# Kernel optimization log

Measured on AMD Instinct MI355X. Metric: run time of the kernel, lower is better.

The kernel has to match this reference:

```python
import jax, jax.numpy as jnp
import numpy as np

N_NODES = 100000
N_EDGES = 1600000
IN_DIM, HID_DIM, OUT_DIM = 128, 64, 64


def setup_inputs() -> dict:
    key = jax.random.key(0)
    ks = jax.random.split(key, 8)
    x = jax.random.normal(ks[0], (N_NODES, IN_DIM), dtype=jnp.float32)
    edge_index = jax.random.randint(ks[1], (2, N_EDGES), 0, N_NODES, dtype=jnp.int32)
    edge_weight = jax.random.uniform(ks[2], (N_EDGES,), dtype=jnp.float32)
    # GCNConv parameters (glorot-ish init)
    w1 = jax.random.normal(ks[3], (IN_DIM, HID_DIM), dtype=jnp.float32) / np.sqrt(IN_DIM)
    b1 = jnp.zeros((HID_DIM,), dtype=jnp.float32)
    w2 = jax.random.normal(ks[4], (HID_DIM, OUT_DIM), dtype=jnp.float32) / np.sqrt(HID_DIM)
    b2 = jnp.zeros((OUT_DIM,), dtype=jnp.float32)
    return {"x": x, "edge_index": edge_index, "edge_weight": edge_weight,
            "w1": w1, "b1": b1, "w2": w2, "b2": b2}


def _gcn_conv(h, src, dst, edge_weight, w, b, n_nodes):
    # GCNConv(normalize=False): linear transform, then edge-weighted scatter-add
    # (source_to_target flow: gather from src, scatter-sum into dst), then bias.
    h = h @ w                                   # [N, out]
    msg = h[src] * edge_weight[:, None]          # [E, out] irregular gather
    agg = jax.ops.segment_sum(msg, dst, num_segments=n_nodes)  # [N, out]
    return agg + b


def reference(x, edge_index, edge_weight, w1, b1, w2, b2):
    src, dst = edge_index[0], edge_index[1]
    n = x.shape[0]
    # Dropout is identity in eval mode (training=False).
    h = _gcn_conv(x, src, dst, edge_weight, w1, b1, n)
    h = jax.nn.relu(h)
    out = _gcn_conv(h, src, dst, edge_weight, w2, b2, n)
    return out
```

## Files before the change

### kernel.cpp

```cpp
#include <hip/hip_runtime.h>
#include <hip/hip_bf16.h>


#define N_NODES 100000
#define N_EDGES 1600000
#define NB1     391
#define T1      3072
#define NT1     521
#define CAP1    4706
#define GB1     782

typedef unsigned short ushort_t;
typedef unsigned int uint_t;
typedef __attribute__((ext_vector_type(8))) short bf16x8;
typedef __attribute__((ext_vector_type(4))) float floatx4;
typedef __attribute__((ext_vector_type(8))) ushort_t ushort8v;

static __device__ __forceinline__ float bf2f(ushort_t h) {
    return __uint_as_float(((uint_t)h) << 16);
}
static __device__ __forceinline__ ushort_t f2bf(float f) {
    uint_t u = __float_as_uint(f);
    u = (u + 0x7FFF + ((u >> 16) & 1)) >> 16;
    return (ushort_t)u;
}

__global__ __launch_bounds__(512) void k_init(int* __restrict__ gcursor)
{
    int t = threadIdx.x;
    if (t < NB1) gcursor[t] = t * CAP1;
}

__global__ __launch_bounds__(512) void k_p1g1(
    const int* __restrict__ src, const int* __restrict__ dst,
    const float* __restrict__ ew, int* __restrict__ gcursor,
    int2* __restrict__ recs1, int E,
    const float* __restrict__ X, const float* __restrict__ W,
    ushort_t* __restrict__ Y, int N)
{
    __shared__ __align__(16) char smem[37056];
    const int tid = threadIdx.x;

    if (blockIdx.x < NT1) {
        int* cnt     = (int*)smem;
        int* start   = cnt + NB1;
        int* cursor  = start + NB1;
        int* gb      = cursor + NB1;
        int* wsum    = (int*)(smem + 6256);
        int* wexc    = wsum + 8;
        int2* stg    = (int2*)(smem + 6336);
        ushort_t* sb = (ushort_t*)(smem + 30912);
        const int t = tid, b = blockIdx.x;
        const int lane = t & 63, wv = t >> 6;

        if (t < NB1) cnt[t] = 0;
        __syncthreads();
        const int e0 = b * T1;
        const int e1 = min(E, e0 + T1);
        for (int e = e0 + t; e < e1; e += 512)
            atomicAdd(&cnt[dst[e] >> 8], 1);
        __syncthreads();

        const int v = (t < NB1) ? cnt[t] : 0;
        int x = v;
        #pragma unroll
        for (int off = 1; off < 64; off <<= 1) {
            int y = __shfl_up(x, off);
            if (lane >= off) x += y;
        }
        if (lane == 63) wsum[wv] = x;
        __syncthreads();
        if (t < 8) {
            int w  = wsum[t];
            int xx = w;
            #pragma unroll
            for (int off = 1; off < 8; off <<= 1) {
                int y = __shfl_up(xx, off);
                if (t >= off) xx += y;
            }
            wexc[t] = xx - w;
        }
        __syncthreads();
        if (t < NB1) {
            int st = x + wexc[wv] - v;
            start[t]  = st;
            cursor[t] = st;
            gb[t]     = atomicAdd(&gcursor[t], v);
        }
        __syncthreads();

        for (int e = e0 + t; e < e1; e += 512) {
            int d  = dst[e];
            int bk = d >> 8;
            int p  = atomicAdd(&cursor[bk], 1);
            int2 r;
            r.x = ((d & 255) << 17) | src[e];
            r.y = __float_as_int(ew[e]);
            stg[p] = r;
            sb[p]  = (ushort_t)bk;
        }
        __syncthreads();
        const int n = e1 - e0;
        for (int i = t; i < n; i += 512) {
            int bk = sb[i];
            recs1[gb[bk] + (i - start[bk])] = stg[i];
        }
    } else {
        ushort_t* sA = (ushort_t*)smem;
        ushort_t* sB = (ushort_t*)(smem + 18432);
        const int b    = blockIdx.x - NT1;
        const int row0 = b * 128;

        for (int i = tid; i < 128 * 16; i += 512) {
            int k = i >> 4, n4 = (i & 15) * 4;
            float4 v = *(const float4*)(W + (size_t)k * 64 + n4);
            sB[(n4 + 0) * 136 + k] = f2bf(v.x);
            sB[(n4 + 1) * 136 + k] = f2bf(v.y);
            sB[(n4 + 2) * 136 + k] = f2bf(v.z);
            sB[(n4 + 3) * 136 + k] = f2bf(v.w);
        }
        for (int i = tid; i < 128 * 16; i += 512) {
            int r = i >> 4, c4 = (i & 15) * 4;
            int rg = row0 + r; if (rg > N - 1) rg = N - 1;
            float4 v = *(const float4*)(X + (size_t)rg * 128 + c4);
            *(ushort4*)(sA + r * 72 + c4) =
                make_ushort4(f2bf(v.x), f2bf(v.y), f2bf(v.z), f2bf(v.w));
        }
        __syncthreads();

        const int wid = tid >> 6, lane = tid & 63;
        const int m = lane & 15, quad = lane >> 4;
        floatx4 acc[4] = {};

        #pragma unroll
        for (int ksl = 0; ksl < 2; ++ksl) {
            bf16x8 a = *(const bf16x8*)(sA + (wid * 16 + m) * 72 + ksl * 32 + quad * 8);
            #pragma unroll
            for (int nt = 0; nt < 4; ++nt) {
                bf16x8 bfr = *(const bf16x8*)(sB + (nt * 16 + m) * 136 + ksl * 32 + quad * 8);
                acc[nt] = __builtin_amdgcn_mfma_f32_16x16x32_bf16(a, bfr, acc[nt], 0, 0, 0);
            }
        }
        __syncthreads();
        for (int i = tid; i < 128 * 16; i += 512) {
            int r = i >> 4, c4 = (i & 15) * 4;
            int rg = row0 + r; if (rg > N - 1) rg = N - 1;
            float4 v = *(const float4*)(X + (size_t)rg * 128 + 64 + c4);
            *(ushort4*)(sA + r * 72 + c4) =
                make_ushort4(f2bf(v.x), f2bf(v.y), f2bf(v.z), f2bf(v.w));
        }
        __syncthreads();
        #pragma unroll
        for (int ksl = 0; ksl < 2; ++ksl) {
            bf16x8 a = *(const bf16x8*)(sA + (wid * 16 + m) * 72 + ksl * 32 + quad * 8);
            #pragma unroll
            for (int nt = 0; nt < 4; ++nt) {
                bf16x8 bfr = *(const bf16x8*)(sB + (nt * 16 + m) * 136 + 64 + ksl * 32 + quad * 8);
                acc[nt] = __builtin_amdgcn_mfma_f32_16x16x32_bf16(a, bfr, acc[nt], 0, 0, 0);
            }
        }
        __syncthreads();
        #pragma unroll
        for (int nt = 0; nt < 4; ++nt)
            #pragma unroll
            for (int r = 0; r < 4; ++r)
                sA[(wid * 16 + quad * 4 + r) * 72 + nt * 16 + m] = f2bf(acc[nt][r]);
        __syncthreads();
        for (int i = tid; i < 128 * 8; i += 512) {
            int rr = i >> 3, c8 = (i & 7) * 8;
            int rg = row0 + rr;
            if (rg < N)
                *(ushort8v*)(Y + (size_t)rg * 64 + c8) =
                    *(const ushort8v*)(sA + rr * 72 + c8);
        }
    }
}

__global__ __launch_bounds__(1024) void k_pass2(
    const int2* __restrict__ recs1, const int* __restrict__ gcursor,
    int2* __restrict__ recs2, int2* __restrict__ nodeinfo, int N)
{
    __shared__ int cnt[256];
    __shared__ int s[256];
    __shared__ int cursor[256];
    const int t = threadIdx.x, b = blockIdx.x;
    const int lo = b * CAP1;
    const int hi = gcursor[b];

    if (t < 256) cnt[t] = 0;
    __syncthreads();
    for (int j = lo + t; j < hi; j += 1024)
        atomicAdd(&cnt[((uint_t)recs1[j].x) >> 17], 1);
    __syncthreads();
    const int v = (t < 256) ? cnt[t] : 0;
    if (t < 256) s[t] = v;
    #pragma unroll
    for (int off = 1; off < 256; off <<= 1) {
        __syncthreads();
        int a = (t >= off && t < 256) ? s[t - off] : 0;
        __syncthreads();
        if (t < 256) s[t] += a;
    }
    __syncthreads();
    if (t < 256) {
        const int stl = s[t] - v;
        cursor[t] = stl;
        const int ng = b * 256 + t;
        if (ng < N) {
            int2 ni; ni.x = lo + stl; ni.y = v;
            nodeinfo[ng] = ni;
        }
    }
    __syncthreads();
    for (int j = lo + t; j < hi; j += 1024) {
        int2 r = recs1[j];
        int dl = ((uint_t)r.x) >> 17;
        int p  = atomicAdd(&cursor[dl], 1);
        int2 o;
        o.x = r.x & 0x1FFFF;
        o.y = r.y;
        recs2[lo + p] = o;
    }
}

__global__ __launch_bounds__(256) void k_gemm2(
    const ushort_t* __restrict__ X, const float* __restrict__ W,
    ushort_t* __restrict__ Y, int N)
{
    __shared__ ushort_t sA[64 * 72];
    __shared__ ushort_t sB[64 * 72];
    const int tid  = threadIdx.x;
    const int row0 = blockIdx.x * 64;

    for (int i = tid; i < 64 * 16; i += 256) {
        int r = i >> 4, c4 = (i & 15) * 4;
        int rg = row0 + r; if (rg > N - 1) rg = N - 1;
        *(ushort4*)(sA + r * 72 + c4) =
            *(const ushort4*)(X + (size_t)rg * 64 + c4);
    }
    for (int i = tid; i < 64 * 16; i += 256) {
        int k = i >> 4, n4 = (i & 15) * 4;
        float4 v = *(const float4*)(W + (size_t)k * 64 + n4);
        sB[(n4 + 0) * 72 + k] = f2bf(v.x);
        sB[(n4 + 1) * 72 + k] = f2bf(v.y);
        sB[(n4 + 2) * 72 + k] = f2bf(v.z);
        sB[(n4 + 3) * 72 + k] = f2bf(v.w);
    }
    __syncthreads();

    const int wid = tid >> 6, lane = tid & 63;
    const int m = lane & 15, quad = lane >> 4;
    floatx4 acc[4] = {};

    #pragma unroll
    for (int ks = 0; ks < 2; ++ks) {
        bf16x8 a = *(const bf16x8*)(sA + (wid * 16 + m) * 72 + ks * 32 + quad * 8);
        #pragma unroll
        for (int nt = 0; nt < 4; ++nt) {
            bf16x8 bfr = *(const bf16x8*)(sB + (nt * 16 + m) * 72 + ks * 32 + quad * 8);
            acc[nt] = __builtin_amdgcn_mfma_f32_16x16x32_bf16(a, bfr, acc[nt], 0, 0, 0);
        }
    }
    __syncthreads();
    #pragma unroll
    for (int nt = 0; nt < 4; ++nt)
        #pragma unroll
        for (int r = 0; r < 4; ++r)
            sA[(wid * 16 + quad * 4 + r) * 72 + nt * 16 + m] = f2bf(acc[nt][r]);
    __syncthreads();
    for (int i = tid; i < 64 * 8; i += 256) {
        int rr = i >> 3, c8 = (i & 7) * 8;
        int rg = row0 + rr;
        if (rg < N)
            *(ushort8v*)(Y + (size_t)rg * 64 + c8) =
                *(const ushort8v*)(sA + rr * 72 + c8);
    }
}

template<bool RELU, bool OUT_BF16>
__global__ __launch_bounds__(256) void k_gather(
    const ushort_t* __restrict__ H, const int2* __restrict__ recs,
    const int2* __restrict__ nodeinfo, const float* __restrict__ bias,
    void* __restrict__ out)
{
    const int wid  = threadIdx.x >> 6;
    const int lane = threadIdx.x & 63;
    const int n0   = (blockIdx.x * 4 + wid) * 2;
    const int n1   = n0 + 1;

    const int2 niA = nodeinfo[n0];
    const int2 niB = nodeinfo[n1];
    int baseA = niA.x; const int endA = niA.x + niA.y;
    int baseB = niB.x; const int endB = niB.x + niB.y;

    const int g  = lane >> 4;
    const int c4 = (lane & 15) * 4;

    float a0 = 0.f, a1 = 0.f, a2 = 0.f, a3 = 0.f;
    float b0 = 0.f, b1 = 0.f, b2 = 0.f, b3 = 0.f;

    while (baseA < endA || baseB < endB) {
        int mA = endA - baseA; if (mA > 64) mA = 64;
        int mB = endB - baseB; if (mB > 64) mB = 64;
        int2 rA = (mA > 0) ? recs[baseA + (lane < mA ? lane : mA - 1)]
                           : make_int2(0, 0);
        int2 rB = (mB > 0) ? recs[baseB + (lane < mB ? lane : mB - 1)]
                           : make_int2(0, 0);
        float wAf = __int_as_float(rA.y);
        float wBf = __int_as_float(rB.y);
        int mm = mA > mB ? mA : mB;
        #pragma unroll 4
        for (int jj = 0; jj < mm; jj += 4) {
            int idx = jj + g;
            int   sA = __shfl(rA.x, idx);
            float wA = __shfl(wAf, idx);
            int   sB = __shfl(rB.x, idx);
            float wB = __shfl(wBf, idx);
            if (idx >= mA) wA = 0.f;
            if (idx >= mB) wB = 0.f;
            ushort4 hA = *(const ushort4*)(H + (size_t)sA * 64 + c4);
            ushort4 hB = *(const ushort4*)(H + (size_t)sB * 64 + c4);
            a0 = fmaf(wA, bf2f(hA.x), a0);
            a1 = fmaf(wA, bf2f(hA.y), a1);
            a2 = fmaf(wA, bf2f(hA.z), a2);
            a3 = fmaf(wA, bf2f(hA.w), a3);
            b0 = fmaf(wB, bf2f(hB.x), b0);
            b1 = fmaf(wB, bf2f(hB.y), b1);
            b2 = fmaf(wB, bf2f(hB.z), b2);
            b3 = fmaf(wB, bf2f(hB.w), b3);
        }
        baseA += 64;
        baseB += 64;
    }
    a0 += __shfl_down(a0, 32); a1 += __shfl_down(a1, 32);
    a2 += __shfl_down(a2, 32); a3 += __shfl_down(a3, 32);
    b0 += __shfl_down(b0, 32); b1 += __shfl_down(b1, 32);
    b2 += __shfl_down(b2, 32); b3 += __shfl_down(b3, 32);
    a0 += __shfl_down(a0, 16); a1 += __shfl_down(a1, 16);
    a2 += __shfl_down(a2, 16); a3 += __shfl_down(a3, 16);
    b0 += __shfl_down(b0, 16); b1 += __shfl_down(b1, 16);
    b2 += __shfl_down(b2, 16); b3 += __shfl_down(b3, 16);

    if (lane < 16) {
        float4 bv = *(const float4*)(bias + c4);
        float vA0 = a0 + bv.x, vA1 = a1 + bv.y, vA2 = a2 + bv.z, vA3 = a3 + bv.w;
        float vB0 = b0 + bv.x, vB1 = b1 + bv.y, vB2 = b2 + bv.z, vB3 = b3 + bv.w;
        if (RELU) {
            vA0 = fmaxf(vA0, 0.f); vA1 = fmaxf(vA1, 0.f);
            vA2 = fmaxf(vA2, 0.f); vA3 = fmaxf(vA3, 0.f);
            vB0 = fmaxf(vB0, 0.f); vB1 = fmaxf(vB1, 0.f);
            vB2 = fmaxf(vB2, 0.f); vB3 = fmaxf(vB3, 0.f);
        }
        if (OUT_BF16) {
            *(ushort4*)((ushort_t*)out + (size_t)n0 * 64 + c4) =
                make_ushort4(f2bf(vA0), f2bf(vA1), f2bf(vA2), f2bf(vA3));
            *(ushort4*)((ushort_t*)out + (size_t)n1 * 64 + c4) =
                make_ushort4(f2bf(vB0), f2bf(vB1), f2bf(vB2), f2bf(vB3));
        } else {
            *(float4*)((float*)out + (size_t)n0 * 64 + c4) =
                make_float4(vA0, vA1, vA2, vA3);
            *(float4*)((float*)out + (size_t)n1 * 64 + c4) =
                make_float4(vB0, vB1, vB2, vB3);
        }
    }
}

extern "C" void kernel_launch(void* const* d_in, const int* in_sizes, int n_in,
                              void* d_out, int out_size, void* d_ws, size_t ws_size,
                              hipStream_t stream) {
    const float* x   = (const float*)d_in[0];
    const int*   ei  = (const int*)  d_in[1];
    const float* ew  = (const float*)d_in[2];
    const float* w1  = (const float*)d_in[3];
    const float* b1  = (const float*)d_in[4];
    const float* w2  = (const float*)d_in[5];
    const float* b2  = (const float*)d_in[6];
    float* out = (float*)d_out;

    const int N = N_NODES, E = N_EDGES;
    const int* src = ei;
    const int* dst = ei + E;

    char* p = (char*)d_ws;
    ushort_t* bufA   = (ushort_t*)p;  p += (size_t)N_NODES * 64 * 2;
    int2*     recs2  = (int2*)p;      p += (size_t)NB1 * CAP1 * 8;
    int2*     recs1  = (int2*)p;
    ushort_t* bufB   = (ushort_t*)p;  p += (size_t)NB1 * CAP1 * 8;
    int*      gcur   = (int*)p;       p += 2048;
    int2*     ninfo  = (int2*)p;      p += (size_t)N_NODES * 8;

    k_init <<<1, 512, 0, stream>>>(gcur);
    k_p1g1 <<<NT1 + GB1, 512, 0, stream>>>(src, dst, ew, gcur, recs1, E,
                                           x, w1, bufA, N);
    k_pass2<<<NB1, 1024, 0, stream>>>(recs1, gcur, recs2, ninfo, N);

    k_gather<true, true><<<N / 8, 256, 0, stream>>>(bufA, recs2, ninfo, b1, bufB);

    k_gemm2<<<(N + 63) / 64, 256, 0, stream>>>(bufB, w2, bufA, N);
    k_gather<false, false><<<N / 8, 256, 0, stream>>>(bufA, recs2, ninfo, b2, out);
}
```

Baseline: 235.6 us.

## Preload edges into registers in binning pass and widen gather loads

The binning kernel now uses larger edge tiles of 4096, so fewer tiles are launched. Each thread preloads 8 edges (dst, src, weight) into registers once, where the old loop read dst twice, once for counting and once for scattering. The gather kernel now has each lane load 8 bf16 values (16 bytes) instead of 4 and issues four independent row loads per batch to raise memory-level parallelism. This costs more registers and shared memory per block, which may lower occupancy.

Result: slower. 255.1 us (+8.3%).

```diff
diff --git a/kernel.cpp b/kernel.cpp
--- a/kernel.cpp
+++ b/kernel.cpp
@@ -5,8 +5,9 @@
 #define N_NODES 100000
 #define N_EDGES 1600000
 #define NB1     391
-#define T1      3072
-#define NT1     521
+#define T1      4096
+#define NT1     391
+#define EPT     8
 #define CAP1    4706
 #define GB1     782
 
@@ -38,7 +39,7 @@
     const float* __restrict__ X, const float* __restrict__ W,
     ushort_t* __restrict__ Y, int N)
 {
-    __shared__ __align__(16) char smem[37056];
+    __shared__ __align__(16) char smem[47296];
     const int tid = threadIdx.x;
 
     if (blockIdx.x < NT1) {
@@ -49,16 +50,28 @@
         int* wsum    = (int*)(smem + 6256);
         int* wexc    = wsum + 8;
         int2* stg    = (int2*)(smem + 6336);
-        ushort_t* sb = (ushort_t*)(smem + 30912);
+        ushort_t* sb = (ushort_t*)(smem + 39104);
         const int t = tid, b = blockIdx.x;
         const int lane = t & 63, wv = t >> 6;
 
-        if (t < NB1) cnt[t] = 0;
-        __syncthreads();
+        int   rd[EPT]; int rs[EPT]; float rw[EPT];
         const int e0 = b * T1;
         const int e1 = min(E, e0 + T1);
-        for (int e = e0 + t; e < e1; e += 512)
-            atomicAdd(&cnt[dst[e] >> 8], 1);
+        #pragma unroll
+        for (int i = 0; i < EPT; ++i) {
+            int e  = e0 + t + i * 512;
+            int ee = (e < e1) ? e : e0;
+            rd[i] = dst[ee];
+            rs[i] = src[ee];
+            rw[i] = ew[ee];
+            if (e >= e1) rd[i] = -1;
+        }
+
+        if (t < NB1) cnt[t] = 0;
+        __syncthreads();
+        #pragma unroll
+        for (int i = 0; i < EPT; ++i)
+            if (rd[i] >= 0) atomicAdd(&cnt[rd[i] >> 8], 1);
         __syncthreads();
 
         const int v = (t < NB1) ? cnt[t] : 0;
@@ -89,15 +102,18 @@
         }
         __syncthreads();
 
-        for (int e = e0 + t; e < e1; e += 512) {
-            int d  = dst[e];
-            int bk = d >> 8;
-            int p  = atomicAdd(&cursor[bk], 1);
-            int2 r;
-            r.x = ((d & 255) << 17) | src[e];
-            r.y = __float_as_int(ew[e]);
-            stg[p] = r;
-            sb[p]  = (ushort_t)bk;
+        #pragma unroll
+        for (int i = 0; i < EPT; ++i) {
+            int d = rd[i];
+            if (d >= 0) {
+                int bk = d >> 8;
+                int p  = atomicAdd(&cursor[bk], 1);
+                int2 r;
+                r.x = ((d & 255) << 17) | rs[i];
+                r.y = __float_as_int(rw[i]);
+                stg[p] = r;
+                sb[p]  = (ushort_t)bk;
+            }
         }
         __syncthreads();
         const int n = e1 - e0;
@@ -293,11 +309,10 @@
     int baseA = niA.x; const int endA = niA.x + niA.y;
     int baseB = niB.x; const int endB = niB.x + niB.y;
 
-    const int g  = lane >> 4;
-    const int c4 = (lane & 15) * 4;
-
-    float a0 = 0.f, a1 = 0.f, a2 = 0.f, a3 = 0.f;
-    float b0 = 0.f, b1 = 0.f, b2 = 0.f, b3 = 0.f;
+    const int g  = lane >> 3;
+    const int c8 = (lane & 7) * 8;
+
+    float accA[8] = {}, accB[8] = {};
 
     while (baseA < endA || baseB < endB) {
         int mA = endA - baseA; if (mA > 64) mA = 64;
@@ -309,58 +324,77 @@
         float wAf = __int_as_float(rA.y);
         float wBf = __int_as_float(rB.y);
         int mm = mA > mB ? mA : mB;
-        #pragma unroll 4
-        for (int jj = 0; jj < mm; jj += 4) {
-            int idx = jj + g;
-            int   sA = __shfl(rA.x, idx);
-            float wA = __shfl(wAf, idx);
-            int   sB = __shfl(rB.x, idx);
-            float wB = __shfl(wBf, idx);
-            if (idx >= mA) wA = 0.f;
-            if (idx >= mB) wB = 0.f;
-            ushort4 hA = *(const ushort4*)(H + (size_t)sA * 64 + c4);
-            ushort4 hB = *(const ushort4*)(H + (size_t)sB * 64 + c4);
-            a0 = fmaf(wA, bf2f(hA.x), a0);
-            a1 = fmaf(wA, bf2f(hA.y), a1);
-            a2 = fmaf(wA, bf2f(hA.z), a2);
-            a3 = fmaf(wA, bf2f(hA.w), a3);
-            b0 = fmaf(wB, bf2f(hB.x), b0);
-            b1 = fmaf(wB, bf2f(hB.y), b1);
-            b2 = fmaf(wB, bf2f(hB.z), b2);
-            b3 = fmaf(wB, bf2f(hB.w), b3);
+
+        #pragma unroll
+        for (int half = 0; half < 2; ++half) {
+            int j0 = half * 32;
+            if (j0 < mm) {
+                ushort8v hA_[4], hB_[4];
+                float    wA_[4], wB_[4];
+                #pragma unroll
+                for (int s = 0; s < 4; ++s) {
+                    int idx = j0 + s * 8 + g;
+                    int   sa = __shfl(rA.x, idx);
+                    float wa = __shfl(wAf, idx);
+                    int   sb = __shfl(rB.x, idx);
+                    float wb = __shfl(wBf, idx);
+                    wA_[s] = (idx < mA) ? wa : 0.f;
+                    wB_[s] = (idx < mB) ? wb : 0.f;
+                    hA_[s] = *(const ushort8v*)(H + (size_t)sa * 64 + c8);
+                    hB_[s] = *(const ushort8v*)(H + (size_t)sb * 64 + c8);
+                }
+                #pragma unroll
+                for (int s = 0; s < 4; ++s) {
+                    #pragma unroll
+                    for (int c = 0; c < 8; ++c) {
+                        accA[c] = fmaf(wA_[s], bf2f(hA_[s][c]), accA[c]);
+                        accB[c] = fmaf(wB_[s], bf2f(hB_[s][c]), accB[c]);
+                    }
+                }
+            }
         }
         baseA += 64;
         baseB += 64;
     }
-    a0 += __shfl_down(a0, 32); a1 += __shfl_down(a1, 32);
-    a2 += __shfl_down(a2, 32); a3 += __shfl_down(a3, 32);
-    b0 += __shfl_down(b0, 32); b1 += __shfl_down(b1, 32);
-    b2 += __shfl_down(b2, 32); b3 += __shfl_down(b3, 32);
-    a0 += __shfl_down(a0, 16); a1 += __shfl_down(a1, 16);
-    a2 += __shfl_down(a2, 16); a3 += __shfl_down(a3, 16);
-    b0 += __shfl_down(b0, 16); b1 += __shfl_down(b1, 16);
-    b2 += __shfl_down(b2, 16); b3 += __shfl_down(b3, 16);
-
-    if (lane < 16) {
-        float4 bv = *(const float4*)(bias + c4);
-        float vA0 = a0 + bv.x, vA1 = a1 + bv.y, vA2 = a2 + bv.z, vA3 = a3 + bv.w;
-        float vB0 = b0 + bv.x, vB1 = b1 + bv.y, vB2 = b2 + bv.z, vB3 = b3 + bv.w;
-        if (RELU) {
-            vA0 = fmaxf(vA0, 0.f); vA1 = fmaxf(vA1, 0.f);
-            vA2 = fmaxf(vA2, 0.f); vA3 = fmaxf(vA3, 0.f);
-            vB0 = fmaxf(vB0, 0.f); vB1 = fmaxf(vB1, 0.f);
-            vB2 = fmaxf(vB2, 0.f); vB3 = fmaxf(vB3, 0.f);
+    #pragma unroll
+    for (int c = 0; c < 8; ++c) {
+        accA[c] += __shfl_down(accA[c], 32);
+        accB[c] += __shfl_down(accB[c], 32);
+    }
+    #pragma unroll
+    for (int c = 0; c < 8; ++c) {
+        accA[c] += __shfl_down(accA[c], 16);
+        accB[c] += __shfl_down(accB[c], 16);
+    }
+    #pragma unroll
+    for (int c = 0; c < 8; ++c) {
+        accA[c] += __shfl_down(accA[c], 8);
+        accB[c] += __shfl_down(accB[c], 8);
+    }
+
+    if (lane < 8) {
+        float bb[8];
+        *(float4*)&bb[0] = *(const float4*)(bias + c8);
+        *(float4*)&bb[4] = *(const float4*)(bias + c8 + 4);
+        float vA[8], vB[8];
+        #pragma unroll
+        for (int c = 0; c < 8; ++c) {
+            vA[c] = accA[c] + bb[c];
+            vB[c] = accB[c] + bb[c];
+            if (RELU) { vA[c] = fmaxf(vA[c], 0.f); vB[c] = fmaxf(vB[c], 0.f); }
         }
         if (OUT_BF16) {
-            *(ushort4*)((ushort_t*)out + (size_t)n0 * 64 + c4) =
-                make_ushort4(f2bf(vA0), f2bf(vA1), f2bf(vA2), f2bf(vA3));
-            *(ushort4*)((ushort_t*)out + (size_t)n1 * 64 + c4) =
-                make_ushort4(f2bf(vB0), f2bf(vB1), f2bf(vB2), f2bf(vB3));
+            ushort8v pa, pb;
+            #pragma unroll
+            for (int c = 0; c < 8; ++c) { pa[c] = f2bf(vA[c]); pb[c] = f2bf(vB[c]); }
+            *(ushort8v*)((ushort_t*)out + (size_t)n0 * 64 + c8) = pa;
+            *(ushort8v*)((ushort_t*)out + (size_t)n1 * 64 + c8) = pb;
         } else {
-            *(float4*)((float*)out + (size_t)n0 * 64 + c4) =
-                make_float4(vA0, vA1, vA2, vA3);
-            *(float4*)((float*)out + (size_t)n1 * 64 + c4) =
-                make_float4(vB0, vB1, vB2, vB3);
+            float* o = (float*)out;
+            *(float4*)(o + (size_t)n0 * 64 + c8)     = make_float4(vA[0], vA[1], vA[2], vA[3]);
+            *(float4*)(o + (size_t)n0 * 64 + c8 + 4) = make_float4(vA[4], vA[5], vA[6], vA[7]);
+            *(float4*)(o + (size_t)n1 * 64 + c8)     = make_float4(vB[0], vB[1], vB[2], vB[3]);
+            *(float4*)(o + (size_t)n1 * 64 + c8 + 4) = make_float4(vB[4], vB[5], vB[6], vB[7]);
         }
     }
 }
```
